# Kernel tuning notes

Measured on AMD Instinct MI355X. Metric: run time of the kernel, lower is better.

The kernel has to match this reference:

```python
import jax, jax.numpy as jnp
import numpy as np

S, B, D, H, NH = 512, 64, 1024, 2048, 8

def setup_inputs() -> dict:
    key = jax.random.key(0)
    k1, k2, k3, k4, k5 = jax.random.split(key, 5)
    input_matrix = jax.random.normal(k1, (S, B, D), dtype=jnp.float32)
    lim_r = 1.0 / np.sqrt(D)
    lim_a = 1.0 / np.sqrt(H)
    W_red = jax.random.uniform(k2, (H, D), minval=-lim_r, maxval=lim_r, dtype=jnp.float32)
    b_red = jax.random.uniform(k3, (H,), minval=-lim_r, maxval=lim_r, dtype=jnp.float32)
    W_att = jax.random.uniform(k4, (NH, H), minval=-lim_a, maxval=lim_a, dtype=jnp.float32)
    b_att = jax.random.uniform(k5, (NH,), minval=-lim_a, maxval=lim_a, dtype=jnp.float32)
    return {"input_matrix": input_matrix, "W_red": W_red, "b_red": b_red, "W_att": W_att, "b_att": b_att}

def reference(input_matrix, W_red, b_red, W_att, b_att):
    # input_matrix: [S, B, D] (seq-first)
    reduced = jnp.einsum('sbd,hd->sbh', input_matrix, W_red) + b_red   # [S,B,H]
    activated = jax.nn.relu(reduced)
    logits = jnp.einsum('sbh,ah->sba', activated, W_att) + b_att       # [S,B,NH]
    attn = jax.nn.softmax(logits, axis=0)                              # softmax over words
    # penalty: || A A^T - I ||_F per batch, summed over batch
    A = jnp.transpose(attn, (1, 0, 2))                                 # [B,S,NH]
    AAt = jnp.einsum('bsa,bta->bst', A, A)                             # [B,S,S]
    diff = AAt - jnp.eye(S, dtype=AAt.dtype)
    penalty = jnp.sum(jnp.sqrt(jnp.sum(diff * diff, axis=(1, 2))))
    # attended vector: sum_s attn[s,b,h] * x[s,b,d] -> [B, NH*D]
    attended = jnp.einsum('sba,sbd->bad', attn, input_matrix).reshape(B, NH * D)
    return attended, penalty
```

## Files before the change

### kernel.cpp

```cpp
#include <hip/hip_runtime.h>
#include <hip/hip_bf16.h>
#include <math.h>

constexpr int kS = 512, kB = 64, kD = 1024, kH = 2048, kNH = 8;
constexpr int kM = kS * kB;

typedef __attribute__((ext_vector_type(8))) short bf16x8;
typedef __attribute__((ext_vector_type(4))) float f32x4;

#define GLB(p) ((const __attribute__((address_space(1))) unsigned int*)(p))
#define LDSP(p) ((__attribute__((address_space(3))) unsigned int*)(p))

__device__ __forceinline__ unsigned short f2bf(float f) {
  unsigned int u = __builtin_bit_cast(unsigned int, f);
  unsigned int r = (u + 0x7fffu + ((u >> 16) & 1u)) >> 16;
  return (unsigned short)r;
}

__global__ __launch_bounds__(256) void cvt_bf16(const float* __restrict__ src,
                                                unsigned short* __restrict__ dst,
                                                int n8) {
  int i = blockIdx.x * 256 + threadIdx.x;
  if (i >= n8) return;
  const float4* s4 = (const float4*)src;
  float4 v0 = s4[2 * i], v1 = s4[2 * i + 1];
  union { unsigned short u[8]; float4 f2[2]; } o;
  o.u[0] = f2bf(v0.x); o.u[1] = f2bf(v0.y); o.u[2] = f2bf(v0.z); o.u[3] = f2bf(v0.w);
  o.u[4] = f2bf(v1.x); o.u[5] = f2bf(v1.y); o.u[6] = f2bf(v1.z); o.u[7] = f2bf(v1.w);
  *(float4*)(dst + (size_t)i * 8) = o.f2[0];
}

__global__ __launch_bounds__(256, 3) void gemm_fused(
    const unsigned short* __restrict__ Abf,
    const unsigned short* __restrict__ Wbf,
    const float* __restrict__ b_red,
    const float* __restrict__ W_att,
    float* __restrict__ logits)
{
  __shared__ union {
    struct { unsigned short Ab[128 * 64]; unsigned short Bb[128 * 64]; } st;
    float et[32 * 132];
  } u;
  __shared__ float Wa[8 * 128];

  const int tid = threadIdx.x;
  const int lane = tid & 63;
  const int w = tid >> 6;
  const int wr = w >> 1, wc = w & 1;

  int bid = blockIdx.x;
  int swz = (bid & 7) * 512 + (bid >> 3);
  const int nt = swz & 15, mt = swz >> 4;
  const int m0 = mt * 128, n0 = nt * 128;

  const unsigned short* gA[4];
  const unsigned short* gB[4];
#pragma unroll
  for (int i = 0; i < 4; ++i) {
    const int ck = w * 4 + i;
    const int row = ck * 8 + (lane >> 3);
    const int srcSlot = (lane & 7) ^ (lane >> 3);
    gA[i] = Abf + (size_t)(m0 + row) * kD + srcSlot * 8;
    gB[i] = Wbf + (size_t)(n0 + row) * kD + srcSlot * 8;
  }

  f32x4 acc[4][4] = {};

  for (int kt = 0; kt < kD / 64; ++kt) {
#pragma unroll
    for (int i = 0; i < 4; ++i) {
      const int ck = w * 4 + i;
      __builtin_amdgcn_global_load_lds(GLB(gA[i]), LDSP(&u.st.Ab[ck * 512 + lane * 8]), 16, 0, 0);
      __builtin_amdgcn_global_load_lds(GLB(gB[i]), LDSP(&u.st.Bb[ck * 512 + lane * 8]), 16, 0, 0);
      gA[i] += 64; gB[i] += 64;
    }
    __syncthreads();

#pragma unroll
    for (int s = 0; s < 2; ++s) {
      const int slot = (s * 4 + (lane >> 4)) ^ (lane & 7);
      bf16x8 aF[4], bF[4];
#pragma unroll
      for (int m = 0; m < 4; ++m) {
        const int row = wr * 64 + m * 16 + (lane & 15);
        aF[m] = *(const bf16x8*)&u.st.Ab[row * 64 + slot * 8];
      }
#pragma unroll
      for (int n = 0; n < 4; ++n) {
        const int row = wc * 64 + n * 16 + (lane & 15);
        bF[n] = *(const bf16x8*)&u.st.Bb[row * 64 + slot * 8];
      }
#pragma unroll
      for (int m = 0; m < 4; ++m)
#pragma unroll
        for (int n = 0; n < 4; ++n)
          acc[m][n] = __builtin_amdgcn_mfma_f32_16x16x32_bf16(aF[m], bF[n], acc[m][n], 0, 0, 0);
    }
    __syncthreads();
  }

  float bias[4];
#pragma unroll
  for (int n = 0; n < 4; ++n) bias[n] = b_red[n0 + wc * 64 + n * 16 + (lane & 15)];

#pragma unroll
  for (int c = 0; c < 4; ++c) {
    if (wr == (c >> 1)) {
#pragma unroll
      for (int m2 = 0; m2 < 2; ++m2) {
        const int m = (c & 1) * 2 + m2;
#pragma unroll
        for (int n = 0; n < 4; ++n) {
          const int colL = wc * 64 + n * 16 + (lane & 15);
#pragma unroll
          for (int j = 0; j < 4; ++j) {
            const int rowL = m2 * 16 + (lane >> 4) * 4 + j;
            float v = acc[m][n][j] + bias[n];
            u.et[rowL * 132 + colL] = v > 0.f ? v : 0.f;
          }
        }
      }
    }
    if (c == 0 && wr == 1) {
      const int t = tid - 128;
#pragma unroll
      for (int a = 0; a < 8; ++a) Wa[a * 128 + t] = W_att[a * kH + n0 + t];
    }
    __syncthreads();

    {
      const int row = tid >> 3;
      const int q = tid & 7;
      float pa[8] = {0.f, 0.f, 0.f, 0.f, 0.f, 0.f, 0.f, 0.f};
#pragma unroll
      for (int i = 0; i < 16; ++i) {
        const int col = q + i * 8;
        const float v = u.et[row * 132 + col];
#pragma unroll
        for (int a = 0; a < 8; ++a) pa[a] += v * Wa[a * 128 + col];
      }
#pragma unroll
      for (int a = 0; a < 8; ++a) {
        pa[a] += __shfl_xor(pa[a], 1);
        pa[a] += __shfl_xor(pa[a], 2);
        pa[a] += __shfl_xor(pa[a], 4);
      }
      if (q == 0) {
        const int gr = m0 + c * 32 + row;
#pragma unroll
        for (int a = 0; a < 8; ++a) atomicAdd(&logits[(size_t)gr * 8 + a], pa[a]);
      }
    }
    __syncthreads();
  }
}

__global__ __launch_bounds__(256) void softmax_pen(const float* __restrict__ logits,
                                                   const float* __restrict__ b_att,
                                                   float* __restrict__ attn,
                                                   float* __restrict__ pen) {
  __shared__ float sm[512 * 8];
  __shared__ float red[256];
  __shared__ float mx[8];
  __shared__ float dn[8];
  const int b = blockIdx.x, t = threadIdx.x;

  float ba[8];
#pragma unroll
  for (int a = 0; a < 8; ++a) ba[a] = b_att[a];

  const float4* lg = (const float4*)(logits + (size_t)b * 8);
  float4* sm4 = (float4*)sm;
#pragma unroll
  for (int i = 0; i < 4; ++i) {
    const int s = t * 2 + (i >> 1), piece = i & 1;
    float4 v = lg[(size_t)s * 128 + piece];
    v.x += ba[piece * 4 + 0]; v.y += ba[piece * 4 + 1];
    v.z += ba[piece * 4 + 2]; v.w += ba[piece * 4 + 3];
    sm4[s * 2 + piece] = v;
  }
  __syncthreads();

  const int a = t & 7, part = t >> 3;
  float m = -1e30f;
  for (int k = 0; k < 16; ++k) m = fmaxf(m, sm[(part + 32 * k) * 8 + a]);
  red[a * 32 + part] = m;
  __syncthreads();
  if (t < 8) {
    float mm = -1e30f;
    for (int p = 0; p < 32; ++p) mm = fmaxf(mm, red[t * 32 + p]);
    mx[t] = mm;
  }
  __syncthreads();

  float ps = 0.f;
  const float mxa = mx[a];
  for (int k = 0; k < 16; ++k) {
    const int idx = (part + 32 * k) * 8 + a;
    const float e = __expf(sm[idx] - mxa);
    sm[idx] = e;
    ps += e;
  }
  red[a * 32 + part] = ps;
  __syncthreads();
  if (t < 8) {
    float ss = 0.f;
    for (int p = 0; p < 32; ++p) ss += red[t * 32 + p];
    dn[t] = 1.f / ss;
  }
  __syncthreads();

  float dv[8];
#pragma unroll
  for (int i = 0; i < 8; ++i) dv[i] = dn[i];
  float4* ao = (float4*)(attn + (size_t)b * 8);
#pragma unroll
  for (int i = 0; i < 4; ++i) {
    const int s = t * 2 + (i >> 1), piece = i & 1;
    float4 v = sm4[s * 2 + piece];
    v.x *= dv[piece * 4 + 0]; v.y *= dv[piece * 4 + 1];
    v.z *= dv[piece * 4 + 2]; v.w *= dv[piece * 4 + 3];
    sm4[s * 2 + piece] = v;
    ao[(size_t)s * 128 + piece] = v;
  }
  __syncthreads();

  if (t < 64) {
    const int ra = t >> 3, rb = t & 7;
    float Mv = 0.f;
    for (int s = 0; s < 512; ++s) Mv += sm[s * 8 + ra] * sm[s * 8 + rb];
    float c = Mv * Mv - (ra == rb ? 2.f * Mv : 0.f);
#pragma unroll
    for (int off = 32; off; off >>= 1) c += __shfl_down(c, off);
    if (t == 0) pen[b] = sqrtf(c + 512.f);
  }
}

__global__ __launch_bounds__(256) void attended_k(const float* __restrict__ attn,
                                                  const float* __restrict__ x,
                                                  float* __restrict__ out) {
  __shared__ float at[512 * 8];
  const int b = blockIdx.x >> 2, dc = blockIdx.x & 3;
  const int t = threadIdx.x;

  const float4* ap = (const float4*)(attn + (size_t)b * 8);
  float4* at4 = (float4*)at;
#pragma unroll
  for (int i = 0; i < 4; ++i) {
    const int s = t * 2 + (i >> 1), piece = i & 1;
    at4[s * 2 + piece] = ap[(size_t)s * 128 + piece];
  }
  __syncthreads();

  const int d = dc * 256 + t;
  const float* xp = x + (size_t)b * kD + d;
  float acc[8] = {0.f, 0.f, 0.f, 0.f, 0.f, 0.f, 0.f, 0.f};
  for (int s0 = 0; s0 < 512; s0 += 4) {
    float xs[4];
#pragma unroll
    for (int ss = 0; ss < 4; ++ss) xs[ss] = xp[(size_t)(s0 + ss) * (kB * kD)];
#pragma unroll
    for (int ss = 0; ss < 4; ++ss) {
      const float4 p0 = at4[(s0 + ss) * 2];
      const float4 p1 = at4[(s0 + ss) * 2 + 1];
      acc[0] += p0.x * xs[ss]; acc[1] += p0.y * xs[ss];
      acc[2] += p0.z * xs[ss]; acc[3] += p0.w * xs[ss];
      acc[4] += p1.x * xs[ss]; acc[5] += p1.y * xs[ss];
      acc[6] += p1.z * xs[ss]; acc[7] += p1.w * xs[ss];
    }
  }
  float* op = out + (size_t)b * (kNH * kD) + d;
#pragma unroll
  for (int a = 0; a < 8; ++a) op[(size_t)a * kD] = acc[a];
}

__global__ void finalize_pen(const float* __restrict__ pen, float* __restrict__ out) {
  const int t = threadIdx.x;
  float v = pen[t];
#pragma unroll
  for (int off = 32; off; off >>= 1) v += __shfl_down(v, off);
  if (t == 0) out[(size_t)kB * kNH * kD] = v;
}

extern "C" void kernel_launch(void* const* d_in, const int* in_sizes, int n_in,
                              void* d_out, int out_size, void* d_ws, size_t ws_size,
                              hipStream_t stream) {
  const float* x     = (const float*)d_in[0];
  const float* W_red = (const float*)d_in[1];
  const float* b_red = (const float*)d_in[2];
  const float* W_att = (const float*)d_in[3];
  const float* b_att = (const float*)d_in[4];
  float* out = (float*)d_out;

  char* ws = (char*)d_ws;
  unsigned short* Abf = (unsigned short*)ws;
  unsigned short* Wbf = (unsigned short*)(ws + (size_t)67108864);
  float* logits = (float*)(ws + (size_t)71303168);
  float* attn   = (float*)(ws + (size_t)72351744);
  float* pen    = (float*)(ws + (size_t)73400320);

  hipMemsetAsync(logits, 0, (size_t)kM * kNH * sizeof(float), stream);

  cvt_bf16<<<16384, 256, 0, stream>>>(x, Abf, (kM * kD) / 8);
  cvt_bf16<<<1024, 256, 0, stream>>>(W_red, Wbf, (kH * kD) / 8);

  gemm_fused<<<4096, 256, 0, stream>>>(Abf, Wbf, b_red, W_att, logits);

  softmax_pen<<<kB, 256, 0, stream>>>(logits, b_att, attn, pen);
  attended_k<<<kB * 4, 256, 0, stream>>>(attn, x, out);
  finalize_pen<<<1, 64, 0, stream>>>(pen, out);
}
```

Measured before the change: 624.4 us.

## Stage GEMM tiles in MFMA fragment order and split Gram reduction across warps

Global loads into shared memory now place each 16-row by 8-column chunk so that each lane's MFMA fragment sits contiguously at lane*8, replacing the XOR-swizzled row layout with fragment-major placement. This removes per-iteration slot/row address arithmetic on the shared-memory reads and is meant to keep them conflict-free. Separately, the 8x8 attention Gram product in the softmax kernel is split across all 256 threads in four partial sums over the sequence, instead of 64 threads each looping over 512 positions. The new global load pattern reads 16 rows by 64 bytes per instruction, which may coalesce less well than the previous contiguous row pattern.

```diff
diff --git a/kernel.cpp b/kernel.cpp
--- a/kernel.cpp
+++ b/kernel.cpp
@@ -58,10 +58,11 @@
 #pragma unroll
   for (int i = 0; i < 4; ++i) {
     const int ck = w * 4 + i;
-    const int row = ck * 8 + (lane >> 3);
-    const int srcSlot = (lane & 7) ^ (lane >> 3);
-    gA[i] = Abf + (size_t)(m0 + row) * kD + srcSlot * 8;
-    gB[i] = Wbf + (size_t)(n0 + row) * kD + srcSlot * 8;
+    const int half = ck >> 3, mfrag = (ck & 7) >> 1, shalf = ck & 1;
+    const int row = half * 64 + mfrag * 16 + (lane & 15);
+    const int col = (shalf * 4 + (lane >> 4)) * 8;
+    gA[i] = Abf + (size_t)(m0 + row) * kD + col;
+    gB[i] = Wbf + (size_t)(n0 + row) * kD + col;
   }
 
   f32x4 acc[4][4] = {};
@@ -78,18 +79,13 @@
 
 #pragma unroll
     for (int s = 0; s < 2; ++s) {
-      const int slot = (s * 4 + (lane >> 4)) ^ (lane & 7);
       bf16x8 aF[4], bF[4];
 #pragma unroll
-      for (int m = 0; m < 4; ++m) {
-        const int row = wr * 64 + m * 16 + (lane & 15);
-        aF[m] = *(const bf16x8*)&u.st.Ab[row * 64 + slot * 8];
-      }
-#pragma unroll
-      for (int n = 0; n < 4; ++n) {
-        const int row = wc * 64 + n * 16 + (lane & 15);
-        bF[n] = *(const bf16x8*)&u.st.Bb[row * 64 + slot * 8];
-      }
+      for (int m = 0; m < 4; ++m)
+        aF[m] = *(const bf16x8*)&u.st.Ab[(wr * 8 + m * 2 + s) * 512 + lane * 8];
+#pragma unroll
+      for (int n = 0; n < 4; ++n)
+        bF[n] = *(const bf16x8*)&u.st.Bb[(wc * 8 + n * 2 + s) * 512 + lane * 8];
 #pragma unroll
       for (int m = 0; m < 4; ++m)
 #pragma unroll
@@ -225,10 +221,18 @@
   }
   __syncthreads();
 
+  {
+    const int pair = t & 63, part4 = t >> 6;
+    const int ra = pair >> 3, rb = pair & 7;
+    float Mv = 0.f;
+    for (int s = part4 * 128; s < part4 * 128 + 128; ++s)
+      Mv += sm[s * 8 + ra] * sm[s * 8 + rb];
+    red[part4 * 64 + pair] = Mv;
+  }
+  __syncthreads();
   if (t < 64) {
     const int ra = t >> 3, rb = t & 7;
-    float Mv = 0.f;
-    for (int s = 0; s < 512; ++s) Mv += sm[s * 8 + ra] * sm[s * 8 + rb];
+    float Mv = red[t] + red[64 + t] + red[128 + t] + red[192 + t];
     float c = Mv * Mv - (ra == rb ? 2.f * Mv : 0.f);
 #pragma unroll
     for (int off = 32; off; off >>= 1) c += __shfl_down(c, off);
```

Result: no change. 632.1 us (+1.2%).
